# Optimization experiments

Hardware: AMD Instinct MI355X
Metric: run time of the kernel (lower is better)

Reference implementation:

```python
import jax, jax.numpy as jnp
import numpy as np
from jax import lax

SIGMA = 1.0
ALPHA = 1.0
BETA = 1.0
TRUNCATE = 4.0  # scipy.ndimage default


def _gauss_kernel(sigma):
    radius = int(TRUNCATE * sigma + 0.5)  # scipy radius rule -> 4 for sigma=1
    x = np.arange(-radius, radius + 1, dtype=np.float64)
    k = np.exp(-0.5 * (x / sigma) ** 2)
    k = (k / k.sum()).astype(np.float32)
    return k

_KERNEL = _gauss_kernel(SIGMA)


def _blur_axis(img, k, axis):
    # scipy mode='reflect' == jnp.pad mode='symmetric' (edge repeated)
    r = len(k) // 2
    pad = [(0, 0)] * img.ndim
    pad[axis] = (r, r)
    xp = jnp.pad(img, pad, mode='symmetric')
    n = img.shape[axis]
    out = k[0] * lax.slice_in_dim(xp, 0, n, axis=axis)
    for i in range(1, len(k)):
        out = out + k[i] * lax.slice_in_dim(xp, i, i + n, axis=axis)
    return out


def gaussian_blur(img):
    # scalar sigma in scipy blurs along EVERY axis, including batch & channel
    k = jnp.asarray(_KERNEL, dtype=img.dtype)
    for ax in range(img.ndim):
        img = _blur_axis(img, k, ax)
    return img


def decompose(I):
    I_log = jnp.log(I + 1e-6)
    I_smooth = gaussian_blur(I_log)
    R = I_log - I_smooth
    L = I_log - R  # == I_smooth
    return jnp.exp(L), jnp.exp(R)


def setup_inputs() -> dict:
    key = jax.random.key(0)
    k1, k2 = jax.random.split(key)
    shape = (16, 3, 512, 512)
    I_enhanced = jax.random.uniform(k1, shape, dtype=jnp.float32)
    I_gt = jax.random.uniform(k2, shape, dtype=jnp.float32)
    return {"I_enhanced": I_enhanced, "I_gt": I_gt}


def reference(I_enhanced, I_gt):
    L_enh, R_enh = decompose(I_enhanced)
    L_gt, R_gt = decompose(I_gt)
    L_reflectance = jnp.mean((R_enh - R_gt) ** 2)
    L_illumination = jnp.mean((L_enh - L_gt) ** 2)
    return ALPHA * L_reflectance + BETA * L_illumination
```

## Files before the change

kernel.cpp:

```cpp
#include <hip/hip_runtime.h>
#include <hip/hip_fp16.h>
#include <cmath>

#define PLANE (512*512)
#define NPLANES 48
#define NEL (48*PLANE)

struct Taps { float k[9]; };
struct CMat { float w[3][3]; };


#define FOLD(r) ((r) < 0 ? (-1 - (r)) : ((r) > 511 ? (1023 - (r)) : (r)))

__device__ __forceinline__ uint swap16(uint x) { return (x >> 16) | (x << 16); }
__device__ __forceinline__ uint align16(uint hiSrc, uint loSrc) {
    return (loSrc >> 16) | (hiSrc << 16);
}

__global__ __launch_bounds__(64, 3)
void k_blur_hw(const float* __restrict__ inE, const float* __restrict__ inG,
               ushort* __restrict__ wsS, float* __restrict__ out, Taps tp)
{
    const int l  = threadIdx.x;
    const int r0 = blockIdx.x * 16;
    const int z  = blockIdx.y;
    if (blockIdx.x == 0 && blockIdx.y == 0 && l == 0) *out = 0.f;
    const float* __restrict__ src = (z < NPLANES) ? (inE + z * PLANE)
                                                  : (inG + (z - NPLANES) * PLANE);
    const int col = 8 * l;

    __half2 kh[9];
#pragma unroll
    for (int t = 0; t < 9; ++t) kh[t] = __float2half2_rn(tp.k[t]);

    uint ring[12][4];

    float4 pA[6], pB[6];
#pragma unroll
    for (int s = 0; s < 6; ++s) {
        const int row = FOLD(r0 - 4 + s);
        pA[s] = *(const float4*)(src + row * 512 + col);
        pB[s] = *(const float4*)(src + row * 512 + col + 4);
    }

    for (int jb = 0; jb < 24; jb += 12) {
#pragma unroll
        for (int u = 0; u < 12; ++u) {
            const int j   = jb + u;
            const int sl6 = u % 6;

            const float4 a = pA[sl6], b = pB[sl6];
            if (j + 6 < 24) {
                const int row = FOLD(r0 + 2 + j);
                pA[sl6] = *(const float4*)(src + row * 512 + col);
                pB[sl6] = *(const float4*)(src + row * 512 + col + 4);
            }

            const float e0 = __logf(a.x + 1e-6f), e1 = __logf(a.y + 1e-6f);
            const float e2 = __logf(a.z + 1e-6f), e3 = __logf(a.w + 1e-6f);
            const float e4 = __logf(b.x + 1e-6f), e5 = __logf(b.y + 1e-6f);
            const float e6 = __logf(b.z + 1e-6f), e7 = __logf(b.w + 1e-6f);
            __half2 h01 = __floats2half2_rn(e0, e1);
            __half2 h23 = __floats2half2_rn(e2, e3);
            __half2 h45 = __floats2half2_rn(e4, e5);
            __half2 h67 = __floats2half2_rn(e6, e7);
            const uint P0 = *(uint*)&h01, P2 = *(uint*)&h23;
            const uint P4 = *(uint*)&h45, P6 = *(uint*)&h67;

            uint U4 = (uint)__shfl_up((int)P4, 1);
            uint U6 = (uint)__shfl_up((int)P6, 1);
            uint D0 = (uint)__shfl_down((int)P0, 1);
            uint D2 = (uint)__shfl_down((int)P2, 1);
            if (l == 0)  { U4 = swap16(P2); U6 = swap16(P0); }
            if (l == 63) { D0 = swap16(P6); D2 = swap16(P4); }
            uint pk[15];
            pk[0] = U4; pk[2] = U6; pk[4] = P0; pk[6] = P2;
            pk[8] = P4; pk[10] = P6; pk[12] = D0; pk[14] = D2;
#pragma unroll
            for (int x = 0; x < 7; ++x) pk[2 * x + 1] = align16(pk[2 * x + 2], pk[2 * x]);

#pragma unroll
            for (int q = 0; q < 4; ++q) {
                __half2 acc = __hmul2(kh[0], *(__half2*)&pk[2 * q]);
#pragma unroll
                for (int t = 1; t < 9; ++t)
                    acc = __hfma2(kh[t], *(__half2*)&pk[2 * q + t], acc);
                ring[u][q] = *(uint*)&acc;
            }

            if (j >= 8) {
                __half2 s0, s1, s2, s3;
                {
                    const int sl = (u + 4) % 12;
                    s0 = __hmul2(kh[0], *(__half2*)&ring[sl][0]);
                    s1 = __hmul2(kh[0], *(__half2*)&ring[sl][1]);
                    s2 = __hmul2(kh[0], *(__half2*)&ring[sl][2]);
                    s3 = __hmul2(kh[0], *(__half2*)&ring[sl][3]);
                }
#pragma unroll
                for (int t = 1; t < 9; ++t) {
                    const int sl = (u + 4 + t) % 12;
                    s0 = __hfma2(kh[t], *(__half2*)&ring[sl][0], s0);
                    s1 = __hfma2(kh[t], *(__half2*)&ring[sl][1], s1);
                    s2 = __hfma2(kh[t], *(__half2*)&ring[sl][2], s2);
                    s3 = __hfma2(kh[t], *(__half2*)&ring[sl][3], s3);
                }
                const int ro = r0 + j - 8;
                ushort* dpS = wsS + ((ro * 96) + z) * 512 + col;
                *(uint4*)dpS = make_uint4(*(uint*)&s0, *(uint*)&s1,
                                          *(uint*)&s2, *(uint*)&s3);
            }
        }
    }
}

__global__ __launch_bounds__(256)
void k_cn_loss(const ushort* __restrict__ wsS,
               const float* __restrict__ inE, const float* __restrict__ inG,
               float* __restrict__ out, Taps tp, CMat cm)
{
    const int tid = threadIdx.x;
    const int P   = blockIdx.x * 256 + tid;
    const int hw0 = P * 2;
    const int h   = hw0 >> 9;
    const int w0  = hw0 & 511;
    const ushort* sbase = wsS + (size_t)(h * 96) * 512 + w0;
    const float* __restrict__ ibE = inE + (size_t)h * 512 + w0;
    const float* __restrict__ ibG = inG + (size_t)h * 512 + w0;

    __half2 k2[9], cw[3][3];
#pragma unroll
    for (int t = 0; t < 9; ++t) k2[t] = __float2half2_rn(tp.k[t]);
#pragma unroll
    for (int i = 0; i < 3; ++i)
#pragma unroll
        for (int j = 0; j < 3; ++j) cw[i][j] = __float2half2_rn(cm.w[i][j]);

    __half2 re[9][3];
    __half2 rg[9][3];

#define LOADRAW(m, uE, uG)                                                     \
    uE[0] = *(const uint*)(sbase + ((m) * 3 + 0) * 512);                       \
    uE[1] = *(const uint*)(sbase + ((m) * 3 + 1) * 512);                       \
    uE[2] = *(const uint*)(sbase + ((m) * 3 + 2) * 512);                       \
    uG[0] = *(const uint*)(sbase + (48 + (m) * 3 + 0) * 512);                  \
    uG[1] = *(const uint*)(sbase + (48 + (m) * 3 + 1) * 512);                  \
    uG[2] = *(const uint*)(sbase + (48 + (m) * 3 + 2) * 512);

#define CBLUR(u, dst)                                                          \
    {                                                                          \
        __half2 v0 = *(__half2*)&u[0];                                         \
        __half2 v1 = *(__half2*)&u[1];                                         \
        __half2 v2 = *(__half2*)&u[2];                                         \
        dst[0] = __hfma2(cw[0][0], v0, __hfma2(cw[0][1], v1, __hmul2(cw[0][2], v2))); \
        dst[1] = __hfma2(cw[1][0], v0, __hfma2(cw[1][1], v1, __hmul2(cw[1][2], v2))); \
        dst[2] = __hfma2(cw[2][0], v0, __hfma2(cw[2][1], v1, __hmul2(cw[2][2], v2))); \
    }

#pragma unroll
    for (int m = 0; m < 4; ++m) {
        uint uE[3], uG[3];
        LOADRAW(m, uE, uG);
        CBLUR(uE, re[m]); CBLUR(uG, rg[m]);
    }
    uint nuE[3], nuG[3];
    LOADRAW(4, nuE, nuG);
    float2 fe[3], fg[3];
#pragma unroll
    for (int c = 0; c < 3; ++c) {
        fe[c] = *(const float2*)(ibE + (size_t)c * PLANE);
        fg[c] = *(const float2*)(ibG + (size_t)c * PLANE);
    }

    float acc = 0.f;
#pragma unroll
    for (int n = 0; n < 16; ++n) {
        float2 nfe[3], nfg[3];
        if (n + 1 < 16) {
#pragma unroll
            for (int c = 0; c < 3; ++c) {
                nfe[c] = *(const float2*)(ibE + (size_t)((n + 1) * 3 + c) * PLANE);
                nfg[c] = *(const float2*)(ibG + (size_t)((n + 1) * 3 + c) * PLANE);
            }
        }
        const int mnew = n + 4;
        if (mnew < 16) {
            CBLUR(nuE, re[mnew % 9]); CBLUR(nuG, rg[mnew % 9]);
            if (mnew + 1 < 16) { LOADRAW(mnew + 1, nuE, nuG); }
        }
#pragma unroll
        for (int c = 0; c < 3; ++c) {
            __half2 se2 = __float2half2_rn(0.f), sg2 = se2;
#pragma unroll
            for (int t = 0; t < 9; ++t) {
                int m = n - 4 + t;
                m = (m < 0) ? (-1 - m) : ((m > 15) ? (31 - m) : m);
                se2 = __hfma2(k2[t], re[m % 9][c], se2);
                sg2 = __hfma2(k2[t], rg[m % 9][c], sg2);
            }
            const float2 sef = __half22float2(se2);
            const float2 sgf = __half22float2(sg2);

            {
                float ee = __expf(-sef.x), eg = __expf(-sgf.x);
                float Re = (fe[c].x + 1e-6f) * ee;
                float Rg = (fg[c].x + 1e-6f) * eg;
                float Le = __builtin_amdgcn_rcpf(ee);
                float Lg = __builtin_amdgcn_rcpf(eg);
                float dr = Re - Rg, dl = Le - Lg;
                acc += dr * dr + dl * dl;
            }
            {
                float ee = __expf(-sef.y), eg = __expf(-sgf.y);
                float Re = (fe[c].y + 1e-6f) * ee;
                float Rg = (fg[c].y + 1e-6f) * eg;
                float Le = __builtin_amdgcn_rcpf(ee);
                float Lg = __builtin_amdgcn_rcpf(eg);
                float dr = Re - Rg, dl = Le - Lg;
                acc += dr * dr + dl * dl;
            }
        }
        if (n + 1 < 16) {
#pragma unroll
            for (int c = 0; c < 3; ++c) { fe[c] = nfe[c]; fg[c] = nfg[c]; }
        }
    }
#undef LOADRAW
#undef CBLUR

    __shared__ float red[256];
    red[tid] = acc;
    __syncthreads();
#pragma unroll
    for (int s = 128; s > 0; s >>= 1) {
        if (tid < s) red[tid] += red[tid + s];
        __syncthreads();
    }
    if (tid == 0) atomicAdd(out, red[0] * (1.0f / (float)NEL));
}

extern "C" void kernel_launch(void* const* d_in, const int* in_sizes, int n_in,
                              void* d_out, int out_size, void* d_ws, size_t ws_size,
                              hipStream_t stream) {
    const float* Ie = (const float*)d_in[0];
    const float* Ig = (const float*)d_in[1];

    Taps tp;
    {
        double kk[9], s = 0.0;
        for (int i = 0; i < 9; ++i) { double x = (double)(i - 4); kk[i] = exp(-0.5 * x * x); s += kk[i]; }
        for (int i = 0; i < 9; ++i) tp.k[i] = (float)(kk[i] / s);
    }

    CMat cm;
    {
        for (int c = 0; c < 3; ++c) {
            cm.w[c][0] = cm.w[c][1] = cm.w[c][2] = 0.f;
            for (int t = 0; t < 9; ++t) {
                int m = c - 4 + t;
                int mm = ((m % 6) + 6) % 6;
                if (mm > 2) mm = 5 - mm;
                cm.w[c][mm] += tp.k[t];
            }
        }
    }

    ushort* wsS = (ushort*)d_ws;

    dim3 g1(32, 96);
    k_blur_hw<<<g1, 64, 0, stream>>>(Ie, Ig, wsS, (float*)d_out, tp);
    k_cn_loss<<<512, 256, 0, stream>>>(wsS, Ie, Ig, (float*)d_out, tp, cm);
}
```

Before: 159.4 us.

## Split blur plane width across two blocks with halo loads and block swizzle

The horizontal-vertical blur kernel now has each 64-lane block cover half a row width (4 columns per lane instead of 8), with explicit halo loads at the internal seam. This doubles the block count, shrinks per-thread register state (ring and prefetch buffers), and raises launch bounds occupancy from 3 to 6. A block-index swizzle spreads consecutive blocks across planes and row groups. The cost is redundant halo loads and logs for the edge lanes, plus extra branching.

```diff
diff --git a/kernel.cpp b/kernel.cpp
--- a/kernel.cpp
+++ b/kernel.cpp
@@ -17,99 +17,105 @@
     return (loSrc >> 16) | (hiSrc << 16);
 }
 
-__global__ __launch_bounds__(64, 3)
+__global__ __launch_bounds__(64, 6)
 void k_blur_hw(const float* __restrict__ inE, const float* __restrict__ inG,
                ushort* __restrict__ wsS, float* __restrict__ out, Taps tp)
 {
-    const int l  = threadIdx.x;
-    const int r0 = blockIdx.x * 16;
-    const int z  = blockIdx.y;
-    if (blockIdx.x == 0 && blockIdx.y == 0 && l == 0) *out = 0.f;
+    const int  l  = threadIdx.x;
+    const uint hw = blockIdx.x;
+    if (hw == 0 && l == 0) *out = 0.f;
+    const uint v  = (hw & 7u) * 768u + (hw >> 3);
+    const int rg = (int)(v & 31u);
+    const int pc = (int)(v >> 5);
+    const int z  = pc >> 1;
+    const int w0 = (pc & 1) * 256;
+    const int r0 = rg * 16;
     const float* __restrict__ src = (z < NPLANES) ? (inE + z * PLANE)
                                                   : (inG + (z - NPLANES) * PLANE);
-    const int col = 8 * l;
+    const int col = w0 + 4 * l;
+
+    const bool haloL   = (l == 0  && w0 != 0);
+    const bool haloR   = (l == 63 && w0 == 0);
+    const bool do_halo = haloL || haloR;
+    const int  hcol    = (l == 0) ? (w0 - 4) : (w0 + 256);
 
     __half2 kh[9];
 #pragma unroll
     for (int t = 0; t < 9; ++t) kh[t] = __float2half2_rn(tp.k[t]);
 
-    uint ring[12][4];
-
-    float4 pA[6], pB[6];
-#pragma unroll
-    for (int s = 0; s < 6; ++s) {
-        const int row = FOLD(r0 - 4 + s);
-        pA[s] = *(const float4*)(src + row * 512 + col);
-        pB[s] = *(const float4*)(src + row * 512 + col + 4);
-    }
-
-    for (int jb = 0; jb < 24; jb += 12) {
-#pragma unroll
-        for (int u = 0; u < 12; ++u) {
-            const int j   = jb + u;
-            const int sl6 = u % 6;
-
-            const float4 a = pA[sl6], b = pB[sl6];
-            if (j + 6 < 24) {
-                const int row = FOLD(r0 + 2 + j);
-                pA[sl6] = *(const float4*)(src + row * 512 + col);
-                pB[sl6] = *(const float4*)(src + row * 512 + col + 4);
-            }
-
-            const float e0 = __logf(a.x + 1e-6f), e1 = __logf(a.y + 1e-6f);
-            const float e2 = __logf(a.z + 1e-6f), e3 = __logf(a.w + 1e-6f);
-            const float e4 = __logf(b.x + 1e-6f), e5 = __logf(b.y + 1e-6f);
-            const float e6 = __logf(b.z + 1e-6f), e7 = __logf(b.w + 1e-6f);
-            __half2 h01 = __floats2half2_rn(e0, e1);
-            __half2 h23 = __floats2half2_rn(e2, e3);
-            __half2 h45 = __floats2half2_rn(e4, e5);
-            __half2 h67 = __floats2half2_rn(e6, e7);
-            const uint P0 = *(uint*)&h01, P2 = *(uint*)&h23;
-            const uint P4 = *(uint*)&h45, P6 = *(uint*)&h67;
-
-            uint U4 = (uint)__shfl_up((int)P4, 1);
-            uint U6 = (uint)__shfl_up((int)P6, 1);
-            uint D0 = (uint)__shfl_down((int)P0, 1);
-            uint D2 = (uint)__shfl_down((int)P2, 1);
-            if (l == 0)  { U4 = swap16(P2); U6 = swap16(P0); }
-            if (l == 63) { D0 = swap16(P6); D2 = swap16(P4); }
-            uint pk[15];
-            pk[0] = U4; pk[2] = U6; pk[4] = P0; pk[6] = P2;
-            pk[8] = P4; pk[10] = P6; pk[12] = D0; pk[14] = D2;
-#pragma unroll
-            for (int x = 0; x < 7; ++x) pk[2 * x + 1] = align16(pk[2 * x + 2], pk[2 * x]);
-
-#pragma unroll
-            for (int q = 0; q < 4; ++q) {
-                __half2 acc = __hmul2(kh[0], *(__half2*)&pk[2 * q]);
-#pragma unroll
-                for (int t = 1; t < 9; ++t)
-                    acc = __hfma2(kh[t], *(__half2*)&pk[2 * q + t], acc);
-                ring[u][q] = *(uint*)&acc;
-            }
-
-            if (j >= 8) {
-                __half2 s0, s1, s2, s3;
-                {
-                    const int sl = (u + 4) % 12;
-                    s0 = __hmul2(kh[0], *(__half2*)&ring[sl][0]);
-                    s1 = __hmul2(kh[0], *(__half2*)&ring[sl][1]);
-                    s2 = __hmul2(kh[0], *(__half2*)&ring[sl][2]);
-                    s3 = __hmul2(kh[0], *(__half2*)&ring[sl][3]);
-                }
-#pragma unroll
-                for (int t = 1; t < 9; ++t) {
-                    const int sl = (u + 4 + t) % 12;
-                    s0 = __hfma2(kh[t], *(__half2*)&ring[sl][0], s0);
-                    s1 = __hfma2(kh[t], *(__half2*)&ring[sl][1], s1);
-                    s2 = __hfma2(kh[t], *(__half2*)&ring[sl][2], s2);
-                    s3 = __hfma2(kh[t], *(__half2*)&ring[sl][3], s3);
-                }
-                const int ro = r0 + j - 8;
-                ushort* dpS = wsS + ((ro * 96) + z) * 512 + col;
-                *(uint4*)dpS = make_uint4(*(uint*)&s0, *(uint*)&s1,
-                                          *(uint*)&s2, *(uint*)&s3);
-            }
+    uint ring[9][2];
+
+    float4 pA[4], pH[2];
+#pragma unroll
+    for (int s = 0; s < 4; ++s)
+        pA[s] = *(const float4*)(src + FOLD(r0 - 4 + s) * 512 + col);
+    pH[0] = pH[1] = make_float4(1.f, 1.f, 1.f, 1.f);
+#pragma unroll
+    for (int s = 0; s < 2; ++s)
+        if (do_halo) pH[s] = *(const float4*)(src + FOLD(r0 - 4 + s) * 512 + hcol);
+
+#pragma unroll
+    for (int j = 0; j < 24; ++j) {
+        const float4 a = pA[j % 4];
+        const float4 hb = pH[j % 2];
+        if (j + 4 < 24)
+            pA[j % 4] = *(const float4*)(src + FOLD(r0 + j) * 512 + col);
+        if (j + 2 < 24 && do_halo)
+            pH[j % 2] = *(const float4*)(src + FOLD(r0 - 2 + j) * 512 + hcol);
+
+        __half2 h01 = __floats2half2_rn(__logf(a.x + 1e-6f), __logf(a.y + 1e-6f));
+        __half2 h23 = __floats2half2_rn(__logf(a.z + 1e-6f), __logf(a.w + 1e-6f));
+        const uint P0 = *(uint*)&h01, P2 = *(uint*)&h23;
+
+        uint H0 = 0, H2 = 0;
+        if (do_halo) {
+            __half2 g01 = __floats2half2_rn(__logf(hb.x + 1e-6f), __logf(hb.y + 1e-6f));
+            __half2 g23 = __floats2half2_rn(__logf(hb.z + 1e-6f), __logf(hb.w + 1e-6f));
+            H0 = *(uint*)&g01; H2 = *(uint*)&g23;
+        }
+
+        uint U0 = (uint)__shfl_up((int)P0, 1);
+        uint U2 = (uint)__shfl_up((int)P2, 1);
+        uint D0 = (uint)__shfl_down((int)P0, 1);
+        uint D2 = (uint)__shfl_down((int)P2, 1);
+        if (l == 0) {
+            if (w0 == 0) { U0 = swap16(P2); U2 = swap16(P0); }
+            else         { U0 = H0;         U2 = H2;         }
+        }
+        if (l == 63) {
+            if (w0 != 0) { D0 = swap16(P2); D2 = swap16(P0); }
+            else         { D0 = H0;         D2 = H2;         }
+        }
+        uint pk[11];
+        pk[0] = U0; pk[2] = U2; pk[4] = P0; pk[6] = P2; pk[8] = D0; pk[10] = D2;
+#pragma unroll
+        for (int x = 0; x < 5; ++x) pk[2 * x + 1] = align16(pk[2 * x + 2], pk[2 * x]);
+
+#pragma unroll
+        for (int q = 0; q < 2; ++q) {
+            __half2 acc = __hmul2(kh[0], *(__half2*)&pk[2 * q]);
+#pragma unroll
+            for (int t = 1; t < 9; ++t)
+                acc = __hfma2(kh[t], *(__half2*)&pk[2 * q + t], acc);
+            ring[j % 9][q] = *(uint*)&acc;
+        }
+
+        if (j >= 8) {
+            __half2 s0, s1;
+            {
+                const int sl = (j - 8) % 9;
+                s0 = __hmul2(kh[0], *(__half2*)&ring[sl][0]);
+                s1 = __hmul2(kh[0], *(__half2*)&ring[sl][1]);
+            }
+#pragma unroll
+            for (int t = 1; t < 9; ++t) {
+                const int sl = (j - 8 + t) % 9;
+                s0 = __hfma2(kh[t], *(__half2*)&ring[sl][0], s0);
+                s1 = __hfma2(kh[t], *(__half2*)&ring[sl][1], s1);
+            }
+            const int ro = r0 + j - 8;
+            ushort* dpS = wsS + ((ro * 96) + z) * 512 + col;
+            *(uint2*)dpS = make_uint2(*(uint*)&s0, *(uint*)&s1);
         }
     }
 }
@@ -267,7 +273,6 @@
 
     ushort* wsS = (ushort*)d_ws;
 
-    dim3 g1(32, 96);
-    k_blur_hw<<<g1, 64, 0, stream>>>(Ie, Ig, wsS, (float*)d_out, tp);
+    k_blur_hw<<<6144, 64, 0, stream>>>(Ie, Ig, wsS, (float*)d_out, tp);
     k_cn_loss<<<512, 256, 0, stream>>>(wsS, Ie, Ig, (float*)d_out, tp, cm);
 }
```

After: 184.9 us. 16.0% more time.
